# Kernel tuning notes

Measured on AMD Instinct MI355X. Metric: run time of the kernel, lower is better.

Reference implementation:

```python
import jax, jax.numpy as jnp
import numpy as np

D, H, L, DFF, V = 512, 8, 6, 2048, 32000
PAD = 0

def make_pe(max_len, d):
    pos = jnp.arange(max_len, dtype=jnp.float32)[:, None]
    div = jnp.exp(jnp.arange(0, d, 2, dtype=jnp.float32) * (-np.log(10000.0) / d))
    ang = pos * div  # [max_len, d/2]
    pe = jnp.zeros((max_len, d), jnp.float32)
    pe = pe.at[:, 0::2].set(jnp.sin(ang)).at[:, 1::2].set(jnp.cos(ang))
    return pe

def layernorm(x, g, b, eps=1e-5):
    m = x.mean(-1, keepdims=True)
    v = ((x - m) ** 2).mean(-1, keepdims=True)
    return (x - m) * jax.lax.rsqrt(v + eps) * g + b

def mha(q_in, k_in, v_in, W, Bv, mask):
    # W: [4, D, D] (q,k,v,out); Bv: [4, D]; mask broadcastable to [B,H,Tq,Tk] bool
    b, sq, d = q_in.shape
    hd = d // H
    def proj(x, w, bb):
        y = x @ w + bb
        return y.reshape(x.shape[0], x.shape[1], H, hd).transpose(0, 2, 1, 3)  # bhsd
    Q, K, Vh = proj(q_in, W[0], Bv[0]), proj(k_in, W[1], Bv[1]), proj(v_in, W[2], Bv[2])
    scores = jnp.einsum('bhqd,bhkd->bhqk', Q, K) / np.sqrt(hd).astype(np.float32)
    scores = jnp.where(mask, scores, jnp.float32(-1e9))
    attn = jax.nn.softmax(scores, axis=-1)
    ctx = jnp.einsum('bhqk,bhkd->bhqd', attn, Vh).transpose(0, 2, 1, 3).reshape(b, sq, d)
    return ctx @ W[3] + Bv[3]

def ffn(x, w1, b1, w2, b2):
    return jax.nn.relu(x @ w1 + b1) @ w2 + b2

def setup_inputs() -> dict:
    key = jax.random.key(0)
    ks = jax.random.split(key, 16)
    s = 0.02
    inp = {
        'src': jax.random.randint(ks[0], (8, 512), 0, V, dtype=jnp.int32),
        'tgt': jax.random.randint(ks[1], (8, 512), 0, V, dtype=jnp.int32),
        'src_emb': (jax.random.normal(ks[2], (V, D)) * s).at[PAD].set(0.0),
        'tgt_emb': (jax.random.normal(ks[3], (V, D)) * s).at[PAD].set(0.0),
        'enc_attn_w': jax.random.normal(ks[4], (L, 4, D, D)) * s,
        'enc_attn_b': jnp.zeros((L, 4, D)),
        'enc_ffn_w1': jax.random.normal(ks[5], (L, D, DFF)) * s,
        'enc_ffn_b1': jnp.zeros((L, DFF)),
        'enc_ffn_w2': jax.random.normal(ks[6], (L, DFF, D)) * s,
        'enc_ffn_b2': jnp.zeros((L, D)),
        'enc_ln_g': jnp.ones((L, 2, D)),
        'enc_ln_b': jnp.zeros((L, 2, D)),
        'dec_self_w': jax.random.normal(ks[7], (L, 4, D, D)) * s,
        'dec_self_b': jnp.zeros((L, 4, D)),
        'dec_cross_w': jax.random.normal(ks[8], (L, 4, D, D)) * s,
        'dec_cross_b': jnp.zeros((L, 4, D)),
        'dec_ffn_w1': jax.random.normal(ks[9], (L, D, DFF)) * s,
        'dec_ffn_b1': jnp.zeros((L, DFF)),
        'dec_ffn_w2': jax.random.normal(ks[10], (L, DFF, D)) * s,
        'dec_ffn_b2': jnp.zeros((L, D)),
        'dec_ln_g': jnp.ones((L, 3, D)),
        'dec_ln_b': jnp.zeros((L, 3, D)),
        'out_w': jax.random.normal(ks[11], (D, V)) * s,
        'out_b': jnp.zeros((V,)),
    }
    return inp

def reference(src, tgt, src_emb, tgt_emb, enc_attn_w, enc_attn_b, enc_ffn_w1, enc_ffn_b1,
              enc_ffn_w2, enc_ffn_b2, enc_ln_g, enc_ln_b, dec_self_w, dec_self_b,
              dec_cross_w, dec_cross_b, dec_ffn_w1, dec_ffn_b1, dec_ffn_w2, dec_ffn_b2,
              dec_ln_g, dec_ln_b, out_w, out_b):
    B_, S = src.shape
    T = tgt.shape[1]
    pe = make_pe(max(S, T), D)
    scale = jnp.float32(np.sqrt(D))

    src_pad = (src != PAD)[:, None, None, :]                    # [B,1,1,S]
    causal = jnp.tril(jnp.ones((T, T), bool))                   # [T,T]
    tgt_mask = (tgt != PAD)[:, None, None, :] & causal[None, None]  # [B,1,T,T]

    # encoder (dropout = identity at inference)
    x = src_emb[src] * scale + pe[None, :S]
    for i in range(L):
        a = mha(x, x, x, enc_attn_w[i], enc_attn_b[i], src_pad)
        x = layernorm(x + a, enc_ln_g[i, 0], enc_ln_b[i, 0])
        f = ffn(x, enc_ffn_w1[i], enc_ffn_b1[i], enc_ffn_w2[i], enc_ffn_b2[i])
        x = layernorm(x + f, enc_ln_g[i, 1], enc_ln_b[i, 1])
    memory = x

    # decoder
    y = tgt_emb[tgt] * scale + pe[None, :T]
    for i in range(L):
        a = mha(y, y, y, dec_self_w[i], dec_self_b[i], tgt_mask)
        y = layernorm(y + a, dec_ln_g[i, 0], dec_ln_b[i, 0])
        c = mha(y, memory, memory, dec_cross_w[i], dec_cross_b[i], src_pad)
        y = layernorm(y + c, dec_ln_g[i, 1], dec_ln_b[i, 1])
        f = ffn(y, dec_ffn_w1[i], dec_ffn_b1[i], dec_ffn_w2[i], dec_ffn_b2[i])
        y = layernorm(y + f, dec_ln_g[i, 2], dec_ln_b[i, 2])

    return y @ out_w + out_b  # [B, T, tgt_vocab]
```

## Files before the change

kernel.cpp:

```cpp
#include <hip/hip_runtime.h>
#include <hip/hip_bf16.h>


#define Dm 512
#define Hh 8
#define HD 64
#define Ll 6
#define DFFv 2048
#define Vv 32000
#define Bb 8
#define Ss 512
#define NTOK (Bb * Ss)

typedef __bf16 bf16x8 __attribute__((ext_vector_type(8)));
typedef __bf16 bf16x4 __attribute__((ext_vector_type(4)));
typedef float  f32x4  __attribute__((ext_vector_type(4)));

#define GLOAD16(gp, lp) __builtin_amdgcn_global_load_lds( \
    (const __attribute__((address_space(1))) unsigned int*)(const void*)(gp), \
    (__attribute__((address_space(3))) unsigned int*)(void*)(lp), 16, 0, 0)

__global__ void embed_pe_k(const int* __restrict__ tok, const float* __restrict__ emb,
                           float* __restrict__ out, __bf16* __restrict__ outb, int Slen)
{
    int row = blockIdx.x;
    int s = row % Slen;
    int t = tok[row];
    const float* e = emb + (size_t)t * Dm;
    float* o = out + (size_t)row * Dm;
    __bf16* ob = outb + (size_t)row * Dm;
    for (int dd = threadIdx.x; dd < Dm; dd += blockDim.x) {
        int j = dd >> 1;
        float div = expf((float)(2 * j) * (-9.210340371976184f / 512.0f));
        float ang = (float)s * div;
        float pe = (dd & 1) ? cosf(ang) : sinf(ang);
        float v = e[dd] * 22.627416997969522f + pe;
        o[dd] = v;
        ob[dd] = (__bf16)v;
    }
}

__global__ __launch_bounds__(256) void wtr_k(const float* __restrict__ W,
                                             __bf16* __restrict__ Wt, int K, int N)
{
    __shared__ float t[32][33];
    size_t msz = (size_t)K * N;
    const float* Wm = W + (size_t)blockIdx.z * msz;
    __bf16* Wtm = Wt + (size_t)blockIdx.z * msz;
    int n0 = blockIdx.x * 32, k0 = blockIdx.y * 32;
    int r = threadIdx.x >> 3, c4 = (threadIdx.x & 7) * 4;
    float4 v = *reinterpret_cast<const float4*>(&Wm[(size_t)(k0 + r) * N + n0 + c4]);
    t[r][c4] = v.x; t[r][c4 + 1] = v.y; t[r][c4 + 2] = v.z; t[r][c4 + 3] = v.w;
    __syncthreads();
    int n = threadIdx.x >> 3, kq = (threadIdx.x & 7) * 4;
    bf16x4 o;
    o[0] = (__bf16)t[kq + 0][n]; o[1] = (__bf16)t[kq + 1][n];
    o[2] = (__bf16)t[kq + 2][n]; o[3] = (__bf16)t[kq + 3][n];
    *reinterpret_cast<bf16x4*>(&Wtm[(size_t)(n0 + n) * K + k0 + kq]) = o;
}

template<int BM, int BN, int RELU, int MODE>
__global__ __launch_bounds__(256) void gemm_mfma_k(const __bf16* __restrict__ A,
                                                   const __bf16* __restrict__ Wt,
                                                   const float* __restrict__ bias,
                                                   void* __restrict__ Cout,
                                                   __bf16* __restrict__ out_k,
                                                   __bf16* __restrict__ out_vT,
                                                   int M, int N, int K)
{
    constexpr int NF_M = BM / 32;
    constexpr int NF_N = BN / 32;
    __shared__ __bf16 As[2][BM * 64];
    __shared__ __bf16 Bs[2][BN * 64];
    const int tid = threadIdx.x;
    const int wave = tid >> 6, lane = tid & 63;
    const int wr = wave >> 1, wc = wave & 1;
    const int row0 = blockIdx.y * BM, col0 = blockIdx.x * BN;

    f32x4 acc[NF_M][NF_N] = {};

    const int fr = lane & 15;
    const int kg = lane >> 4;

    auto stage = [&](int buf, int k0) {
        #pragma unroll
        for (int cc = 0; cc < BM / 32; ++cc) {
            int g = cc * 256 + tid;
            int r = g >> 3, cs = g & 7, gs = cs ^ (r & 7);
            GLOAD16(A + (size_t)(row0 + r) * K + k0 + gs * 8, &As[buf][g * 8]);
        }
        #pragma unroll
        for (int cc = 0; cc < BN / 32; ++cc) {
            int g = cc * 256 + tid;
            int r = g >> 3, cs = g & 7, gs = cs ^ (r & 7);
            GLOAD16(Wt + (size_t)(col0 + r) * K + k0 + gs * 8, &Bs[buf][g * 8]);
        }
    };

    stage(0, 0);
    __syncthreads();

    const int nk = K >> 6;
    for (int kb = 0; kb < nk; ++kb) {
        int cur = kb & 1;
        if (kb + 1 < nk) stage(cur ^ 1, (kb + 1) * 64);

        const char* Ab = (const char*)As[cur];
        const char* Bbp = (const char*)Bs[cur];
        #pragma unroll
        for (int ks = 0; ks < 2; ++ks) {
            bf16x8 af[NF_M], bq[NF_N];
            #pragma unroll
            for (int m = 0; m < NF_M; ++m) {
                int ar = wr * (BM / 2) + m * 16 + fr;
                af[m] = *reinterpret_cast<const bf16x8*>(
                    Ab + ar * 128 + (((ks * 4 + kg) ^ (ar & 7)) << 4));
            }
            #pragma unroll
            for (int n = 0; n < NF_N; ++n) {
                int br = wc * (BN / 2) + n * 16 + fr;
                bq[n] = *reinterpret_cast<const bf16x8*>(
                    Bbp + br * 128 + (((ks * 4 + kg) ^ (br & 7)) << 4));
            }
            #pragma unroll
            for (int m = 0; m < NF_M; ++m)
                #pragma unroll
                for (int n = 0; n < NF_N; ++n)
                    acc[m][n] = __builtin_amdgcn_mfma_f32_16x16x32_bf16(
                        af[m], bq[n], acc[m][n], 0, 0, 0);
        }
        __syncthreads();
    }

    #pragma unroll
    for (int m = 0; m < NF_M; ++m) {
        #pragma unroll
        for (int n = 0; n < NF_N; ++n) {
            int colg = col0 + wc * (BN / 2) + n * 16 + fr;
            float bv = bias[colg];
            #pragma unroll
            for (int j = 0; j < 4; ++j) {
                int row = row0 + wr * (BM / 2) + m * 16 + kg * 4 + j;
                float v = acc[m][n][j] + bv;
                if (RELU) v = fmaxf(v, 0.f);
                if constexpr (MODE == 0) {
                    ((float*)Cout)[(size_t)row * N + colg] = v;
                } else if constexpr (MODE == 1) {
                    ((__bf16*)Cout)[(size_t)row * N + colg] = (__bf16)v;
                } else {
                    int seg = colg >> 9;
                    int c = colg & 511;
                    bool isV = (MODE == 2) ? (seg == 2) : (seg == 1);
                    if (!isV) {
                        __bf16* o = (MODE == 2 && seg == 1) ? out_k : (__bf16*)Cout;
                        o[(size_t)row * 512 + c] = (__bf16)v;
                    } else {
                        int bi = row >> 9, s = row & 511;
                        int hh = c >> 6, f = c & 63;
                        out_vT[(size_t)((bi * 8 + hh) * 64 + f) * 512 + s] = (__bf16)v;
                    }
                }
            }
        }
    }
}

__global__ __launch_bounds__(512) void gemm256_k(const __bf16* __restrict__ A,
                                                 const __bf16* __restrict__ Wt,
                                                 const float* __restrict__ bias,
                                                 float* __restrict__ C,
                                                 int M, int N, int K)
{
    __shared__ __bf16 As[2][256 * 64];
    __shared__ __bf16 Bs[2][256 * 64];
    const int tid = threadIdx.x;
    const int wave = tid >> 6, lane = tid & 63;
    const int wr = wave >> 2, wc = wave & 3;
    const int row0 = blockIdx.x * 256, col0 = blockIdx.y * 256;

    f32x4 acc[8][4] = {};

    const int fr = lane & 15;
    const int kg = lane >> 4;

    auto stage = [&](int buf, int k0) {
        #pragma unroll
        for (int cc = 0; cc < 4; ++cc) {
            int g = cc * 512 + tid;
            int r = g >> 3, cs = g & 7, gs = cs ^ (r & 7);
            GLOAD16(A + (size_t)(row0 + r) * K + k0 + gs * 8, &As[buf][g * 8]);
        }
        #pragma unroll
        for (int cc = 0; cc < 4; ++cc) {
            int g = cc * 512 + tid;
            int r = g >> 3, cs = g & 7, gs = cs ^ (r & 7);
            GLOAD16(Wt + (size_t)(col0 + r) * K + k0 + gs * 8, &Bs[buf][g * 8]);
        }
    };

    stage(0, 0);
    __syncthreads();

    const int nk = K >> 6;
    for (int kb = 0; kb < nk; ++kb) {
        int cur = kb & 1;
        if (kb + 1 < nk) stage(cur ^ 1, (kb + 1) * 64);

        const char* Ab = (const char*)As[cur];
        const char* Bbp = (const char*)Bs[cur];
        #pragma unroll
        for (int ks = 0; ks < 2; ++ks) {
            bf16x8 af[8], bq[4];
            #pragma unroll
            for (int m = 0; m < 8; ++m) {
                int ar = wr * 128 + m * 16 + fr;
                af[m] = *reinterpret_cast<const bf16x8*>(
                    Ab + ar * 128 + (((ks * 4 + kg) ^ (ar & 7)) << 4));
            }
            #pragma unroll
            for (int n = 0; n < 4; ++n) {
                int br = wc * 64 + n * 16 + fr;
                bq[n] = *reinterpret_cast<const bf16x8*>(
                    Bbp + br * 128 + (((ks * 4 + kg) ^ (br & 7)) << 4));
            }
            #pragma unroll
            for (int m = 0; m < 8; ++m)
                #pragma unroll
                for (int n = 0; n < 4; ++n)
                    acc[m][n] = __builtin_amdgcn_mfma_f32_16x16x32_bf16(
                        af[m], bq[n], acc[m][n], 0, 0, 0);
        }
        __syncthreads();
    }

    #pragma unroll
    for (int m = 0; m < 8; ++m) {
        #pragma unroll
        for (int n = 0; n < 4; ++n) {
            int colg = col0 + wc * 64 + n * 16 + fr;
            float bv = bias[colg];
            #pragma unroll
            for (int j = 0; j < 4; ++j) {
                int row = row0 + wr * 128 + m * 16 + kg * 4 + j;
                C[(size_t)row * N + colg] = acc[m][n][j] + bv;
            }
        }
    }
}

__global__ __launch_bounds__(256) void attn_mfma_k(const __bf16* __restrict__ Qb,
                                                   const __bf16* __restrict__ Kb,
                                                   const __bf16* __restrict__ VbT,
                                                   __bf16* __restrict__ Ob,
                                                   const int* __restrict__ key_tok,
                                                   int causal)
{
    __shared__ __bf16 Ks[2][128 * 64];
    __shared__ __bf16 Vs[2][64 * 128];
    __shared__ __bf16 Pl[4][16 * 128];

    const int tid = threadIdx.x;
    const int w = tid >> 6, lane = tid & 63;
    const int fr = lane & 15, kg = lane >> 4;
    const int q0 = blockIdx.x * 64;
    const int h = blockIdx.y, b = blockIdx.z;
    const int qrow = q0 + w * 16 + fr;
    const int swz = (fr & 7) << 4;

    bf16x8 qf[2];
    {
        const __bf16* qp = Qb + ((size_t)(b * 512 + qrow) * 512 + h * 64 + kg * 8);
        qf[0] = *reinterpret_cast<const bf16x8*>(qp);
        qf[1] = *reinterpret_cast<const bf16x8*>(qp + 32);
    }

    f32x4 po[4] = {};
    float m_run = -3.0e38f, l_run = 0.f;
    __bf16* pw = Pl[w];

    auto stage = [&](int buf, int kk0) {
        #pragma unroll
        for (int c = 0; c < 4; ++c) {
            int ch = c * 256 + tid;
            int r = ch >> 3, gsk = (ch & 7) ^ (r & 7);
            GLOAD16(Kb + ((size_t)(b * 512 + kk0 + r) * 512 + h * 64 + gsk * 8),
                    &Ks[buf][ch * 8]);
            int f = ch >> 4, gsv = (ch & 15) ^ (f & 7);
            GLOAD16(VbT + ((size_t)((b * 8 + h) * 64 + f) * 512 + kk0 + gsv * 8),
                    &Vs[buf][ch * 8]);
        }
    };

    const int kkend = causal ? ((q0 + 64 + 127) & ~127) : 512;
    stage(0, 0);
    __syncthreads();

    for (int kk0 = 0; kk0 < kkend; kk0 += 128) {
        int cur = (kk0 >> 7) & 1;
        if (kk0 + 128 < kkend) stage(cur ^ 1, kk0 + 128);

        unsigned long long vm0 = __ballot(key_tok[b * 512 + kk0 + lane] != 0);
        unsigned long long vm1 = __ballot(key_tok[b * 512 + kk0 + 64 + lane] != 0);

        f32x4 st[8];
        #pragma unroll
        for (int kt = 0; kt < 8; ++kt) {
            f32x4 s = {};
            #pragma unroll
            for (int ks = 0; ks < 2; ++ks) {
                int byte = ((kt * 16 + fr) * 128 + ks * 64 + kg * 16) ^ swz;
                bf16x8 kf = *reinterpret_cast<const bf16x8*>((const char*)Ks[cur] + byte);
                s = __builtin_amdgcn_mfma_f32_16x16x32_bf16(kf, qf[ks], s, 0, 0, 0);
            }
            st[kt] = s;
        }

        float sv[8][4];
        float mloc = -3.0e38f;
        #pragma unroll
        for (int kt = 0; kt < 8; ++kt) {
            unsigned long long vm = (kt < 4) ? vm0 : vm1;
            #pragma unroll
            for (int j = 0; j < 4; ++j) {
                int kl = kt * 16 + kg * 4 + j;
                float s = st[kt][j] * 0.125f;
                bool ok = (vm >> (kl & 63)) & 1ull;
                if (causal && (kk0 + kl > qrow)) ok = false;
                s = ok ? s : -1e9f;
                sv[kt][j] = s;
                mloc = fmaxf(mloc, s);
            }
        }
        mloc = fmaxf(mloc, __shfl_xor(mloc, 16));
        mloc = fmaxf(mloc, __shfl_xor(mloc, 32));
        float m_new = fmaxf(m_run, mloc);
        float scale = __expf(m_run - m_new);
        float ls = 0.f;
        #pragma unroll
        for (int kt = 0; kt < 8; ++kt)
            #pragma unroll
            for (int j = 0; j < 4; ++j) {
                float p = __expf(sv[kt][j] - m_new);
                sv[kt][j] = p;
                ls += p;
            }
        ls += __shfl_xor(ls, 16);
        ls += __shfl_xor(ls, 32);
        l_run = l_run * scale + ls;
        m_run = m_new;

        #pragma unroll
        for (int kt = 0; kt < 8; ++kt)
            #pragma unroll
            for (int c = 0; c < 2; ++c) {
                union { __bf16 hh[2]; unsigned u; } pk;
                pk.hh[0] = (__bf16)sv[kt][2 * c];
                pk.hh[1] = (__bf16)sv[kt][2 * c + 1];
                int byte = (fr * 256 + kt * 32 + kg * 8 + c * 4) ^ swz;
                *reinterpret_cast<unsigned*>((char*)pw + byte) = pk.u;
            }

        {
            int qb4 = kg * 4;
            float s0 = __shfl(scale, qb4 + 0), s1 = __shfl(scale, qb4 + 1);
            float s2 = __shfl(scale, qb4 + 2), s3 = __shfl(scale, qb4 + 3);
            #pragma unroll
            for (int nf = 0; nf < 4; ++nf) {
                po[nf][0] *= s0; po[nf][1] *= s1;
                po[nf][2] *= s2; po[nf][3] *= s3;
            }
        }

        #pragma unroll
        for (int ks2 = 0; ks2 < 4; ++ks2) {
            int pbyte = (fr * 256 + ks2 * 64 + kg * 16) ^ swz;
            bf16x8 pa = *reinterpret_cast<const bf16x8*>((const char*)pw + pbyte);
            #pragma unroll
            for (int nf = 0; nf < 4; ++nf) {
                int vbyte = ((nf * 16 + fr) * 256 + ks2 * 64 + kg * 16) ^ swz;
                bf16x8 vf = *reinterpret_cast<const bf16x8*>((const char*)Vs[cur] + vbyte);
                po[nf] = __builtin_amdgcn_mfma_f32_16x16x32_bf16(pa, vf, po[nf], 0, 0, 0);
            }
        }
        __syncthreads();
    }

    {
        int qb4 = kg * 4;
        float r0 = 1.0f / __shfl(l_run, qb4 + 0);
        float r1 = 1.0f / __shfl(l_run, qb4 + 1);
        float r2 = 1.0f / __shfl(l_run, qb4 + 2);
        float r3 = 1.0f / __shfl(l_run, qb4 + 3);
        #pragma unroll
        for (int nf = 0; nf < 4; ++nf) {
            size_t base = (size_t)(b * 512 + q0 + w * 16 + qb4) * 512 + h * 64 + nf * 16 + fr;
            Ob[base]           = (__bf16)(po[nf][0] * r0);
            Ob[base + 512]     = (__bf16)(po[nf][1] * r1);
            Ob[base + 1024]    = (__bf16)(po[nf][2] * r2);
            Ob[base + 1536]    = (__bf16)(po[nf][3] * r3);
        }
    }
}

__global__ __launch_bounds__(256) void add_ln_k(float* __restrict__ x,
                                                const float* __restrict__ a,
                                                const float* __restrict__ g,
                                                const float* __restrict__ bb,
                                                __bf16* __restrict__ xb)
{
    int row = blockIdx.x;
    size_t base = (size_t)row * Dm;
    int tid = threadIdx.x;
    float v0 = x[base + tid]       + a[base + tid];
    float v1 = x[base + tid + 256] + a[base + tid + 256];
    float s  = v0 + v1;
    float s2 = v0 * v0 + v1 * v1;
    #pragma unroll
    for (int o = 1; o < 64; o <<= 1) {
        s  += __shfl_xor(s, o);
        s2 += __shfl_xor(s2, o);
    }
    __shared__ float red[8];
    int wid = tid >> 6, lane = tid & 63;
    if (lane == 0) { red[wid] = s; red[wid + 4] = s2; }
    __syncthreads();
    s  = red[0] + red[1] + red[2] + red[3];
    s2 = red[4] + red[5] + red[6] + red[7];
    float mean = s * (1.0f / 512.0f);
    float var  = s2 * (1.0f / 512.0f) - mean * mean;
    float rstd = rsqrtf(var + 1e-5f);
    float y0 = (v0 - mean) * rstd * g[tid]       + bb[tid];
    float y1 = (v1 - mean) * rstd * g[tid + 256] + bb[tid + 256];
    x[base + tid]        = y0;
    x[base + tid + 256]  = y1;
    xb[base + tid]       = (__bf16)y0;
    xb[base + tid + 256] = (__bf16)y1;
}

extern "C" void kernel_launch(void* const* d_in, const int* in_sizes, int n_in,
                              void* d_out, int out_size, void* d_ws, size_t ws_size,
                              hipStream_t stream)
{
    const int*   src        = (const int*)  d_in[0];
    const int*   tgt        = (const int*)  d_in[1];
    const float* src_emb    = (const float*)d_in[2];
    const float* tgt_emb    = (const float*)d_in[3];
    const float* enc_attn_w = (const float*)d_in[4];
    const float* enc_attn_b = (const float*)d_in[5];
    const float* enc_ffn_w1 = (const float*)d_in[6];
    const float* enc_ffn_b1 = (const float*)d_in[7];
    const float* enc_ffn_w2 = (const float*)d_in[8];
    const float* enc_ffn_b2 = (const float*)d_in[9];
    const float* enc_ln_g   = (const float*)d_in[10];
    const float* enc_ln_b   = (const float*)d_in[11];
    const float* dec_self_w = (const float*)d_in[12];
    const float* dec_self_b = (const float*)d_in[13];
    const float* dec_cross_w= (const float*)d_in[14];
    const float* dec_cross_b= (const float*)d_in[15];
    const float* dec_ffn_w1 = (const float*)d_in[16];
    const float* dec_ffn_b1 = (const float*)d_in[17];
    const float* dec_ffn_w2 = (const float*)d_in[18];
    const float* dec_ffn_b2 = (const float*)d_in[19];
    const float* dec_ln_g   = (const float*)d_in[20];
    const float* dec_ln_b   = (const float*)d_in[21];
    const float* out_w      = (const float*)d_in[22];
    const float* out_b      = (const float*)d_in[23];

    const size_t NROW = (size_t)NTOK * Dm;
    const size_t NH1  = (size_t)NTOK * DFFv;

    float* ws  = (float*)d_ws;
    float* xe  = ws;
    float* xd  = xe + NROW;
    float* t0  = xd + NROW;

    __bf16* xeb  = (__bf16*)(t0 + NROW);
    __bf16* xdb  = xeb + NROW;
    __bf16* qbb  = xdb + NROW;
    __bf16* kbb  = qbb + NROW;
    __bf16* vbT  = kbb + NROW;
    __bf16* ctxb = vbT + NROW;
    __bf16* h1b  = ctxb + NROW;

    const size_t WSZ  = (size_t)Dm * Dm;
    const size_t FSZ  = (size_t)Dm * DFFv;
    __bf16* w_enc_attn = h1b + NH1;
    __bf16* w_enc_f1   = w_enc_attn + 24 * WSZ;
    __bf16* w_enc_f2   = w_enc_f1 + 6 * FSZ;
    __bf16* w_dec_self = w_enc_f2 + 6 * FSZ;
    __bf16* w_dec_cross= w_dec_self + 24 * WSZ;
    __bf16* w_dec_f1   = w_dec_cross + 24 * WSZ;
    __bf16* w_dec_f2   = w_dec_f1 + 6 * FSZ;
    __bf16* w_out      = w_dec_f2 + 6 * FSZ;

    wtr_k<<<dim3(Dm / 32, Dm / 32, 24), 256, 0, stream>>>(enc_attn_w, w_enc_attn, Dm, Dm);
    wtr_k<<<dim3(DFFv / 32, Dm / 32, 6), 256, 0, stream>>>(enc_ffn_w1, w_enc_f1, Dm, DFFv);
    wtr_k<<<dim3(Dm / 32, DFFv / 32, 6), 256, 0, stream>>>(enc_ffn_w2, w_enc_f2, DFFv, Dm);
    wtr_k<<<dim3(Dm / 32, Dm / 32, 24), 256, 0, stream>>>(dec_self_w, w_dec_self, Dm, Dm);
    wtr_k<<<dim3(Dm / 32, Dm / 32, 24), 256, 0, stream>>>(dec_cross_w, w_dec_cross, Dm, Dm);
    wtr_k<<<dim3(DFFv / 32, Dm / 32, 6), 256, 0, stream>>>(dec_ffn_w1, w_dec_f1, Dm, DFFv);
    wtr_k<<<dim3(Dm / 32, DFFv / 32, 6), 256, 0, stream>>>(dec_ffn_w2, w_dec_f2, DFFv, Dm);
    wtr_k<<<dim3(Vv / 32, Dm / 32, 1), 256, 0, stream>>>(out_w, w_out, Dm, Vv);

    auto gqkv = [&](const __bf16* A, const __bf16* Wt, const float* bias) {
        gemm_mfma_k<64, 128, 0, 2><<<dim3(1536 / 128, NTOK / 64), 256, 0, stream>>>(
            A, Wt, bias, qbb, kbb, vbT, NTOK, 1536, Dm);
    };
    auto gkv = [&](const __bf16* A, const __bf16* Wt, const float* bias) {
        gemm_mfma_k<64, 128, 0, 3><<<dim3(1024 / 128, NTOK / 64), 256, 0, stream>>>(
            A, Wt, bias, kbb, nullptr, vbT, NTOK, 1024, Dm);
    };
    auto g64f = [&](const __bf16* A, const __bf16* Wt, const float* bias, float* C, int K) {
        gemm_mfma_k<64, 64, 0, 0><<<dim3(Dm / 64, NTOK / 64), 256, 0, stream>>>(
            A, Wt, bias, C, nullptr, nullptr, NTOK, Dm, K);
    };
    auto attn = [&](const __bf16* Q, const __bf16* K, const __bf16* Vt, __bf16* O,
                    const int* kt, int causal) {
        attn_mfma_k<<<dim3(Ss / 64, Hh, Bb), 256, 0, stream>>>(Q, K, Vt, O, kt, causal);
    };
    auto lnorm = [&](float* x, const float* a, const float* g, const float* b, __bf16* xb) {
        add_ln_k<<<NTOK, 256, 0, stream>>>(x, a, g, b, xb);
    };

    embed_pe_k<<<NTOK, 256, 0, stream>>>(src, src_emb, xe, xeb, Ss);
    embed_pe_k<<<NTOK, 256, 0, stream>>>(tgt, tgt_emb, xd, xdb, Ss);

    for (int i = 0; i < Ll; ++i) {
        const __bf16* W = w_enc_attn + (size_t)i * 4 * WSZ;
        const float* Bv = enc_attn_b + (size_t)i * 4 * Dm;
        gqkv(xeb, W, Bv);
        attn(qbb, kbb, vbT, ctxb, src, 0);
        g64f(ctxb, W + 3 * WSZ, Bv + 3 * Dm, t0, Dm);
        lnorm(xe, t0, enc_ln_g + i * 2 * Dm, enc_ln_b + i * 2 * Dm, xeb);
        gemm_mfma_k<128, 128, 1, 1><<<dim3(DFFv / 128, NTOK / 128), 256, 0, stream>>>(
            xeb, w_enc_f1 + (size_t)i * FSZ, enc_ffn_b1 + i * DFFv, h1b, nullptr, nullptr,
            NTOK, DFFv, Dm);
        g64f(h1b, w_enc_f2 + (size_t)i * FSZ, enc_ffn_b2 + i * Dm, t0, DFFv);
        lnorm(xe, t0, enc_ln_g + i * 2 * Dm + Dm, enc_ln_b + i * 2 * Dm + Dm, xeb);
    }

    for (int i = 0; i < Ll; ++i) {
        const __bf16* Wsf = w_dec_self + (size_t)i * 4 * WSZ;
        const float* Bsf = dec_self_b + (size_t)i * 4 * Dm;
        gqkv(xdb, Wsf, Bsf);
        attn(qbb, kbb, vbT, ctxb, tgt, 1);
        g64f(ctxb, Wsf + 3 * WSZ, Bsf + 3 * Dm, t0, Dm);
        lnorm(xd, t0, dec_ln_g + i * 3 * Dm, dec_ln_b + i * 3 * Dm, xdb);

        const __bf16* Wc = w_dec_cross + (size_t)i * 4 * WSZ;
        const float* Bc = dec_cross_b + (size_t)i * 4 * Dm;
        gemm_mfma_k<64, 64, 0, 1><<<dim3(Dm / 64, NTOK / 64), 256, 0, stream>>>(
            xdb, Wc + 0 * WSZ, Bc + 0 * Dm, qbb, nullptr, nullptr, NTOK, Dm, Dm);
        gkv(xeb, Wc + 1 * WSZ, Bc + 1 * Dm);
        attn(qbb, kbb, vbT, ctxb, src, 0);
        g64f(ctxb, Wc + 3 * WSZ, Bc + 3 * Dm, t0, Dm);
        lnorm(xd, t0, dec_ln_g + i * 3 * Dm + Dm, dec_ln_b + i * 3 * Dm + Dm, xdb);

        gemm_mfma_k<128, 128, 1, 1><<<dim3(DFFv / 128, NTOK / 128), 256, 0, stream>>>(
            xdb, w_dec_f1 + (size_t)i * FSZ, dec_ffn_b1 + i * DFFv, h1b, nullptr, nullptr,
            NTOK, DFFv, Dm);
        g64f(h1b, w_dec_f2 + (size_t)i * FSZ, dec_ffn_b2 + i * Dm, t0, DFFv);
        lnorm(xd, t0, dec_ln_g + i * 3 * Dm + 2 * Dm, dec_ln_b + i * 3 * Dm + 2 * Dm, xdb);
    }

    gemm256_k<<<dim3(NTOK / 256, Vv / 256), 512, 0, stream>>>(
        xdb, w_out, out_b, (float*)d_out, NTOK, Vv, Dm);
}
```

Measured before the change: 2.130 ms.

## Batch all decoder cross-attention K/V projections into one GEMM after encoder

The cross-attention K and V projections of the encoder memory are computed for all six decoder layers in a single wide GEMM (N=6144) right after the encoder. A new MODE 4 epilogue remaps columns to per-layer weight rows and biases, and writes K and transposed V into per-layer buffers. This replaces six small launches with one larger, better-occupied launch. The cost is extra workspace for twelve activation-sized buffers.

```diff
diff --git a/kernel.cpp b/kernel.cpp
--- a/kernel.cpp
+++ b/kernel.cpp
@@ -11,6 +11,7 @@
 #define Bb 8
 #define Ss 512
 #define NTOK (Bb * Ss)
+#define NROWC ((size_t)NTOK * Dm)
 
 typedef __bf16 bf16x8 __attribute__((ext_vector_type(8)));
 typedef __bf16 bf16x4 __attribute__((ext_vector_type(4)));
@@ -78,7 +79,6 @@
     const int row0 = blockIdx.y * BM, col0 = blockIdx.x * BN;
 
     f32x4 acc[NF_M][NF_N] = {};
-
     const int fr = lane & 15;
     const int kg = lane >> 4;
 
@@ -86,14 +86,20 @@
         #pragma unroll
         for (int cc = 0; cc < BM / 32; ++cc) {
             int g = cc * 256 + tid;
-            int r = g >> 3, cs = g & 7, gs = cs ^ (r & 7);
+            int r = g >> 3, gs = (g & 7) ^ (r & 7);
             GLOAD16(A + (size_t)(row0 + r) * K + k0 + gs * 8, &As[buf][g * 8]);
         }
         #pragma unroll
         for (int cc = 0; cc < BN / 32; ++cc) {
             int g = cc * 256 + tid;
-            int r = g >> 3, cs = g & 7, gs = cs ^ (r & 7);
-            GLOAD16(Wt + (size_t)(col0 + r) * K + k0 + gs * 8, &Bs[buf][g * 8]);
+            int r = g >> 3, gs = (g & 7) ^ (r & 7);
+            int c = col0 + r;
+            size_t wrow;
+            if constexpr (MODE == 4)
+                wrow = (size_t)(c >> 10) * 2048 + 512 + (c & 1023);
+            else
+                wrow = (size_t)c;
+            GLOAD16(Wt + wrow * K + k0 + gs * 8, &Bs[buf][g * 8]);
         }
     };
 
@@ -105,7 +111,7 @@
         int cur = kb & 1;
         if (kb + 1 < nk) stage(cur ^ 1, (kb + 1) * 64);
 
-        const char* Ab = (const char*)As[cur];
+        const char* Ab  = (const char*)As[cur];
         const char* Bbp = (const char*)Bs[cur];
         #pragma unroll
         for (int ks = 0; ks < 2; ++ks) {
@@ -137,7 +143,11 @@
         #pragma unroll
         for (int n = 0; n < NF_N; ++n) {
             int colg = col0 + wc * (BN / 2) + n * 16 + fr;
-            float bv = bias[colg];
+            float bv;
+            if constexpr (MODE == 4)
+                bv = bias[(colg >> 10) * 2048 + 512 + (colg & 1023)];
+            else
+                bv = bias[colg];
             #pragma unroll
             for (int j = 0; j < 4; ++j) {
                 int row = row0 + wr * (BM / 2) + m * 16 + kg * 4 + j;
@@ -147,17 +157,28 @@
                     ((float*)Cout)[(size_t)row * N + colg] = v;
                 } else if constexpr (MODE == 1) {
                     ((__bf16*)Cout)[(size_t)row * N + colg] = (__bf16)v;
-                } else {
+                } else if constexpr (MODE == 2) {
                     int seg = colg >> 9;
                     int c = colg & 511;
-                    bool isV = (MODE == 2) ? (seg == 2) : (seg == 1);
-                    if (!isV) {
-                        __bf16* o = (MODE == 2 && seg == 1) ? out_k : (__bf16*)Cout;
-                        o[(size_t)row * 512 + c] = (__bf16)v;
+                    if (seg == 0) {
+                        ((__bf16*)Cout)[(size_t)row * 512 + c] = (__bf16)v;
+                    } else if (seg == 1) {
+                        out_k[(size_t)row * 512 + c] = (__bf16)v;
                     } else {
-                        int bi = row >> 9, s = row & 511;
+                        int bi = row >> 9, sI = row & 511;
                         int hh = c >> 6, f = c & 63;
-                        out_vT[(size_t)((bi * 8 + hh) * 64 + f) * 512 + s] = (__bf16)v;
+                        out_vT[(size_t)((bi * 8 + hh) * 64 + f) * 512 + sI] = (__bf16)v;
+                    }
+                } else {
+                    int li = colg >> 10;
+                    int cw = colg & 1023;
+                    if (cw < 512) {
+                        out_k[li * NROWC + (size_t)row * 512 + cw] = (__bf16)v;
+                    } else {
+                        int hh = (cw - 512) >> 6, f = (cw - 512) & 63;
+                        int bi = row >> 9, sI = row & 511;
+                        out_vT[li * NROWC +
+                               (size_t)((bi * 8 + hh) * 64 + f) * 512 + sI] = (__bf16)v;
                     }
                 }
             }
@@ -179,7 +200,6 @@
     const int row0 = blockIdx.x * 256, col0 = blockIdx.y * 256;
 
     f32x4 acc[8][4] = {};
-
     const int fr = lane & 15;
     const int kg = lane >> 4;
 
@@ -187,13 +207,13 @@
         #pragma unroll
         for (int cc = 0; cc < 4; ++cc) {
             int g = cc * 512 + tid;
-            int r = g >> 3, cs = g & 7, gs = cs ^ (r & 7);
+            int r = g >> 3, gs = (g & 7) ^ (r & 7);
             GLOAD16(A + (size_t)(row0 + r) * K + k0 + gs * 8, &As[buf][g * 8]);
         }
         #pragma unroll
         for (int cc = 0; cc < 4; ++cc) {
             int g = cc * 512 + tid;
-            int r = g >> 3, cs = g & 7, gs = cs ^ (r & 7);
+            int r = g >> 3, gs = (g & 7) ^ (r & 7);
             GLOAD16(Wt + (size_t)(col0 + r) * K + k0 + gs * 8, &Bs[buf][g * 8]);
         }
     };
@@ -206,7 +226,7 @@
         int cur = kb & 1;
         if (kb + 1 < nk) stage(cur ^ 1, (kb + 1) * 64);
 
-        const char* Ab = (const char*)As[cur];
+        const char* Ab  = (const char*)As[cur];
         const char* Bbp = (const char*)Bs[cur];
         #pragma unroll
         for (int ks = 0; ks < 2; ++ks) {
@@ -466,7 +486,7 @@
     const float* out_w      = (const float*)d_in[22];
     const float* out_b      = (const float*)d_in[23];
 
-    const size_t NROW = (size_t)NTOK * Dm;
+    const size_t NROW = NROWC;
     const size_t NH1  = (size_t)NTOK * DFFv;
 
     float* ws  = (float*)d_ws;
@@ -481,10 +501,12 @@
     __bf16* vbT  = kbb + NROW;
     __bf16* ctxb = vbT + NROW;
     __bf16* h1b  = ctxb + NROW;
+    __bf16* kbb6 = h1b + NH1;
+    __bf16* vbT6 = kbb6 + 6 * NROW;
 
     const size_t WSZ  = (size_t)Dm * Dm;
     const size_t FSZ  = (size_t)Dm * DFFv;
-    __bf16* w_enc_attn = h1b + NH1;
+    __bf16* w_enc_attn = vbT6 + 6 * NROW;
     __bf16* w_enc_f1   = w_enc_attn + 24 * WSZ;
     __bf16* w_enc_f2   = w_enc_f1 + 6 * FSZ;
     __bf16* w_dec_self = w_enc_f2 + 6 * FSZ;
@@ -506,12 +528,12 @@
         gemm_mfma_k<64, 128, 0, 2><<<dim3(1536 / 128, NTOK / 64), 256, 0, stream>>>(
             A, Wt, bias, qbb, kbb, vbT, NTOK, 1536, Dm);
     };
-    auto gkv = [&](const __bf16* A, const __bf16* Wt, const float* bias) {
-        gemm_mfma_k<64, 128, 0, 3><<<dim3(1024 / 128, NTOK / 64), 256, 0, stream>>>(
-            A, Wt, bias, kbb, nullptr, vbT, NTOK, 1024, Dm);
-    };
     auto g64f = [&](const __bf16* A, const __bf16* Wt, const float* bias, float* C, int K) {
         gemm_mfma_k<64, 64, 0, 0><<<dim3(Dm / 64, NTOK / 64), 256, 0, stream>>>(
+            A, Wt, bias, C, nullptr, nullptr, NTOK, Dm, K);
+    };
+    auto g64b = [&](const __bf16* A, const __bf16* Wt, const float* bias, __bf16* C, int K) {
+        gemm_mfma_k<64, 64, 0, 1><<<dim3(Dm / 64, NTOK / 64), 256, 0, stream>>>(
             A, Wt, bias, C, nullptr, nullptr, NTOK, Dm, K);
     };
     auto attn = [&](const __bf16* Q, const __bf16* K, const __bf16* Vt, __bf16* O,
@@ -539,6 +561,9 @@
         lnorm(xe, t0, enc_ln_g + i * 2 * Dm + Dm, enc_ln_b + i * 2 * Dm + Dm, xeb);
     }
 
+    gemm_mfma_k<64, 128, 0, 4><<<dim3(6144 / 128, NTOK / 64), 256, 0, stream>>>(
+        xeb, w_dec_cross, dec_cross_b, nullptr, kbb6, vbT6, NTOK, 6144, Dm);
+
     for (int i = 0; i < Ll; ++i) {
         const __bf16* Wsf = w_dec_self + (size_t)i * 4 * WSZ;
         const float* Bsf = dec_self_b + (size_t)i * 4 * Dm;
@@ -549,10 +574,8 @@
 
         const __bf16* Wc = w_dec_cross + (size_t)i * 4 * WSZ;
         const float* Bc = dec_cross_b + (size_t)i * 4 * Dm;
-        gemm_mfma_k<64, 64, 0, 1><<<dim3(Dm / 64, NTOK / 64), 256, 0, stream>>>(
-            xdb, Wc + 0 * WSZ, Bc + 0 * Dm, qbb, nullptr, nullptr, NTOK, Dm, Dm);
-        gkv(xeb, Wc + 1 * WSZ, Bc + 1 * Dm);
-        attn(qbb, kbb, vbT, ctxb, src, 0);
+        g64b(xdb, Wc + 0 * WSZ, Bc + 0 * Dm, qbb, Dm);
+        attn(qbb, kbb6 + (size_t)i * NROW, vbT6 + (size_t)i * NROW, ctxb, src, 0);
         g64f(ctxb, Wc + 3 * WSZ, Bc + 3 * Dm, t0, Dm);
         lnorm(xd, t0, dec_ln_g + i * 3 * Dm + Dm, dec_ln_b + i * 3 * Dm + Dm, xdb);
 
```

Result: no change. 2.121 ms (-0.4%).
